# Optimization experiments

Measured on AMD Instinct MI355X. Metric: run time of the kernel, lower is better.

The kernel has to match this reference:

```python
import jax, jax.numpy as jnp
import numpy as np
import math

B = 2048
INPUT_SIZE = 1024
OUTPUT_SIZE = 512
SPONGE = 1024
ACT = 256
REC = 256
STORE = ACT + REC  # 512
DEPTH = 8
BDEPTH = 10
NEUTRAL_C = 1.0
SQRT2 = math.sqrt(2.0)


def _make_structure():
    # Deterministic stand-in for the module's random.sample-based recall wiring.
    rng = np.random.RandomState(0)
    half = (SPONGE + 1) // 2
    shuffle_perm = np.array([i // 2 + (i % 2) * half for i in range(SPONGE)], dtype=np.int64)
    unused = []
    recall = []
    for i in range(DEPTH):
        unused.extend(range(i * STORE, (i + 1) * STORE))
        sel = rng.choice(len(unused), size=REC, replace=False)
        sel_set = set(sel.tolist())
        recall.append([unused[k] for k in sorted(sel_set)])
        unused = [u for k, u in enumerate(unused) if k not in sel_set]
    out_mem = np.array(sorted(unused), dtype=np.int64)  # 2048 leftover memory columns
    bf_size = len(out_mem) + SPONGE  # 3072
    bf_depth = int(math.ceil(math.log2(bf_size)))  # 12
    bf_half = (bf_size + 1) // 2
    bf_perm = np.array([i // 2 + (i % 2) * bf_half for i in range(bf_size)], dtype=np.int64)
    return shuffle_perm, np.array(recall, dtype=np.int64), out_mem, bf_perm, bf_size, bf_depth


def setup_inputs() -> dict:
    key = jax.random.key(0)
    ks = jax.random.split(key, 6)
    shuffle_perm, recall_idx, out_mem_idx, bf_perm, bf_size, bf_depth = _make_structure()
    return {
        "X": jax.random.normal(ks[0], (B, INPUT_SIZE), jnp.float32),
        "scales": jnp.ones((INPUT_SIZE,), jnp.float32),
        "angles": jax.random.uniform(ks[1], (DEPTH, BDEPTH, SPONGE // 2), jnp.float32) * (2 * math.pi),
        "act_bias": jax.random.normal(ks[2], (DEPTH, ACT), jnp.float32),
        "act_activation": jax.random.normal(ks[3], (DEPTH, ACT), jnp.float32),
        "act_curvature": jax.random.normal(ks[4], (DEPTH, ACT), jnp.float32),
        "bf_angles": jax.random.uniform(ks[5], (bf_depth, bf_size // 2), jnp.float32) * (2 * math.pi),
        "shuffle_perm": jnp.asarray(shuffle_perm),
        "recall_idx": jnp.asarray(recall_idx),
        "output_mem_idx": jnp.asarray(out_mem_idx),
        "bf_perm": jnp.asarray(bf_perm),
    }


def _base_activation(x, c):
    # In the source, `a` is overwritten with torch.tensor(1.0), so a == 1.
    t = (math.pi / 4) / c
    y0 = (1.0 / c) * (1.0 / SQRT2 - math.cos(math.pi / 2))  # = 1/(c*sqrt(2))
    m0 = math.sin(math.pi / 2)  # = 1
    y1 = (1.0 / c) * (1.0 / SQRT2 - 1.0)
    m1 = math.sin(0.0)  # = 0
    mid = (1.0 / c) * (1.0 / SQRT2 - jnp.cos(math.pi / 4 + c * x))
    return jnp.where(x > t, y0 + m0 * (x - t), jnp.where(x < -t, y1 + m1 * (x + t), mid))


def _butterfly(x, angles, perm):
    # angles: [n_layers, exch]; shuffle -> Givens rotation per pair, extra passthrough
    exch = angles.shape[1]
    for j in range(angles.shape[0]):
        s = x[:, perm]
        x1, x2 = s[:, :exch], s[:, exch:2 * exch]
        ca, sa = jnp.cos(angles[j]), jnp.sin(angles[j])
        x = jnp.concatenate([ca * x1 + sa * x2, -sa * x1 + ca * x2, s[:, 2 * exch:]], axis=1)
    return x


def reference(X, scales, angles, act_bias, act_activation, act_curvature, bf_angles,
              shuffle_perm, recall_idx, output_mem_idx, bf_perm):
    Xs = X * scales
    sponge = Xs[:, :SPONGE]  # input_size == sponge_size: no zero pad, memory[0] is empty
    mem = jnp.zeros((Xs.shape[0], DEPTH * STORE), Xs.dtype)
    for i in range(DEPTH):
        sponge = _butterfly(sponge, angles[i], shuffle_perm)
        x1 = sponge[:, STORE:STORE + ACT] + act_bias[i]  # activation_position == store_size
        c = 0.5 * NEUTRAL_C * (act_curvature[i] + jnp.sqrt(act_curvature[i] ** 2 + 1.0))
        ap = _base_activation(x1, c)
        am = _base_activation(-x1, c)
        act_out = jnp.stack([ap, am], axis=2).reshape(ap.shape[0], 2 * ACT)  # interleave +/-
        mem = mem.at[:, i * STORE:(i + 1) * STORE].set(sponge[:, :STORE])
        recall = mem[:, recall_idx[i]]  # indices only address already-filled columns
        # [act_out | sponge[store:act_pos] (empty) | sponge[act_pos+ACT:] | recall]
        sponge = jnp.concatenate([act_out, sponge[:, STORE + ACT:], recall], axis=1)
    pre = jnp.concatenate([mem[:, output_mem_idx], sponge], axis=1)  # [B, 3072]
    out = _butterfly(pre, bf_angles, bf_perm)
    return out[:, :OUTPUT_SIZE]
```

## Files before the change

kernel.cpp:

```cpp
#include <hip/hip_runtime.h>
#include <math.h>

#define NB 2048
#define DEPTH 8

#define FTAB_OFF    0
#define BF01_OFF    81920
#define BFF_OFF     88064
#define ACT4_OFF    98304
#define PHYSA_OFF   106496
#define PHYSR_OFF   110592
#define PHYSO2_OFF  112640

#define MB0 4608
#define MB1 6656

__global__ void setup_kernel(const float* __restrict__ angles,
                             const float* __restrict__ bf_angles,
                             const float* __restrict__ act_bias,
                             const float* __restrict__ act_curv,
                             const int* __restrict__ recall_idx,
                             const int* __restrict__ out_mem_idx,
                             float* __restrict__ ws) {
    __shared__ int physL[4096];
    if (blockIdx.x < 200) {
        int id = blockIdx.x * 256 + threadIdx.x;
        if (id < 40960) {
            int w = id & 3, t = (id >> 2) & 255, dg = id >> 10;
            int d = dg / 5, g = dg - 5 * d;
            int a = 2 * (t & 127) + (t >> 7);
            int pair = (w == 0) ? a : (w == 1) ? (a + 256)
                     : (w == 2) ? (2 * a) : (2 * a + 1);
            int st = 2 * g + (w >> 1);
            float ang = angles[(d * 10 + st) * 512 + pair];
            float s, c; __sincosf(ang, &s, &c);
            ws[FTAB_OFF + 2 * id]     = c;
            ws[FTAB_OFF + 2 * id + 1] = s;
        } else if (id < 44032) {
            int e = id - 40960;
            int w = e & 3; int ti = e >> 2;
            int t = ti / 3; int i = ti - 3 * t;
            int a = t + 256 * i;
            int pair = (w == 0) ? a : (w == 1) ? (a + 768)
                     : (w == 2) ? (2 * a) : (2 * a + 1);
            int stage = (w < 2) ? 0 : 1;
            float ang = bf_angles[stage * 1536 + pair];
            float s, c; __sincosf(ang, &s, &c);
            ws[BF01_OFF + 2 * e]     = c;
            ws[BF01_OFF + 2 * e + 1] = s;
        } else if (id < 49152) {
            int e = id - 44032;
            int f = e >> 10; int rem = e & 1023; int t = rem >> 2; int w = rem & 3;
            int P;
            if (f == 0) P = 3 * t;
            else if (f < 4) { int k = 8 - 2 * f;
                              P = ((t >> (2 * f)) * (768 >> k)) + (t & ((256 >> k) - 1)); }
            else P = t;
            int pair = (w == 0) ? P : (w == 1) ? (P + 768)
                     : (w == 2) ? (2 * P) : (2 * P + 1);
            int stage = (w < 2) ? (2 + 2 * f) : (3 + 2 * f);
            float ang = bf_angles[stage * 1536 + pair];
            float s, c; __sincosf(ang, &s, &c);
            ws[BFF_OFF + 2 * e]     = c;
            ws[BFF_OFF + 2 * e + 1] = s;
        } else if (id < 51200) {
            int ida = id - 49152;
            float cu = act_curv[ida];
            float c  = 0.5f * (cu + sqrtf(cu * cu + 1.0f));
            ((float4*)(ws + ACT4_OFF))[ida] =
                make_float4(act_bias[ida], c, 1.0f / c, 0.0f);
        }
    } else {
        int tid = threadIdx.x;
        for (int e = tid; e < 4096; e += 256) {
            int v = e, p;
            for (;;) {
                int d = v >> 9, j = v & 511;
                if (d == 0)  { p = j; break; }
                if (j < 256) { p = 256 + d * 256 + j; break; }
                v = recall_idx[(d - 1) * 256 + (j - 256)];
            }
            physL[e] = p;
        }
        __syncthreads();
        int* pa = (int*)(ws + PHYSA_OFF);
        for (int e = tid; e < 2048; e += 256) {
            int d = e >> 8, t = e & 255;
            int a = 2 * (t & 127) + (t >> 7);
            pa[2 * e]     = 2 * physL[d * 512 + 2 * a];
            pa[2 * e + 1] = 2 * physL[d * 512 + 2 * a + 1];
        }
        int* pr = (int*)(ws + PHYSR_OFF);
        for (int e = tid; e < 2048; e += 256)
            pr[e] = 2 * physL[recall_idx[e]];
        int* po = (int*)(ws + PHYSO2_OFF);
        for (int e = tid; e < 3072; e += 256) {
            int tt = e / 12; int r = e - 12 * tt; int i = r >> 2; int k = r & 3;
            int a = tt + 256 * i;
            int tl2 = a >> 1, th2 = a & 1;
            int pos = tl2 + 1536 * th2 + 384 * k;
            po[e] = (pos < 2048) ? 2 * physL[out_mem_idx[pos]]
                                 : MB0 + 2 * (pos - 2048);
        }
    }
}

__device__ __forceinline__ float actf(float x, float c, float ic) {
    const float is2 = 0.70710678118654752f;
    float tt = 0.78539816339744831f * ic;
    float y0 = is2 * ic;
    float y1 = (is2 - 1.0f) * ic;
    float mid = ic * (is2 - __cosf(0.78539816339744831f + c * x));
    return x > tt ? (y0 + (x - tt)) : (x < -tt ? y1 : mid);
}

__launch_bounds__(256, 4)
__global__ void sponge_kernel(const float* __restrict__ X,
                              const float* __restrict__ scales,
                              const float* __restrict__ ws,
                              float* __restrict__ out) {
    __shared__ float L[8704];
    const int t = threadIdx.x;
    const int rowA = blockIdx.x * 2;

    const float4* bf01  = (const float4*)(ws + BF01_OFF);
    const float4* bff   = (const float4*)(ws + BFF_OFF);
    const float4* act4  = (const float4*)(ws + ACT4_OFF);
    const int2* physA  = (const int2*)(ws + PHYSA_OFF);
    const int*  physr  = (const int*)(ws + PHYSR_OFF);
    const int*  physo2 = (const int*)(ws + PHYSO2_OFF);

    const int tl = t & 127, th = t >> 7;
    const int b  = tl + th * 512;
    const int a  = 2 * tl + th;
    const int Wb = 2 * (tl & 15) + 32 * th + 64 * (tl >> 4);
    const int Rb = (tl & 1) + 2 * ((tl >> 2) & 15) + 32 * ((tl >> 1) & 1)
                 + 64 * (tl >> 6) + 512 * th;
    const int WI = 2 * Wb;
    const int RI = 2 * Rb;
    const int u  = t - 128;

    float hA0, hA1, hA2, hA3, hB0, hB1, hB2, hB3;
    {
        const float* Xr0 = X + (size_t)rowA * 1024;
        const float* Xr1 = Xr0 + 1024;
        float s0 = scales[b],       s1 = scales[b + 128];
        float s2 = scales[b + 256], s3 = scales[b + 384];
        hA0 = Xr0[b] * s0; hA1 = Xr0[b + 128] * s1;
        hA2 = Xr0[b + 256] * s2; hA3 = Xr0[b + 384] * s3;
        hB0 = Xr1[b] * s0; hB1 = Xr1[b + 128] * s1;
        hB2 = Xr1[b + 256] * s2; hB3 = Xr1[b + 384] * s3;
    }

    int woff = MB0, roff = MB1;
    const float4* ft = (const float4*)(ws + FTAB_OFF) + 2 * t;

#define DQUAD(cA, cB, i0, i1, i2, i3, F0, F1, F2, F3)                    \
    { float g0 =  (cA).x * (i0) + (cA).y * (i2);                         \
      float g2 = -(cA).y * (i0) + (cA).x * (i2);                         \
      float g1 =  (cA).z * (i1) + (cA).w * (i3);                         \
      float g3 = -(cA).w * (i1) + (cA).z * (i3);                         \
      F0 =  (cB).x * g0 + (cB).y * g1;                                   \
      F2 = -(cB).y * g0 + (cB).x * g1;                                   \
      F1 =  (cB).z * g2 + (cB).w * g3;                                   \
      F3 = -(cB).w * g2 + (cB).z * g3; }

    for (int d = 0; d < DEPTH; ++d) {
        for (int g = 0; g < 5; ++g) {
            float4 csA = ft[0], csB = ft[1]; ft += 512;
            float fA0, fA1, fA2, fA3, fB0, fB1, fB2, fB3;
            DQUAD(csA, csB, hA0, hA1, hA2, hA3, fA0, fA1, fA2, fA3);
            DQUAD(csA, csB, hB0, hB1, hB2, hB3, fB0, fB1, fB2, fB3);
            if (g < 4) {
                *(float4*)(L + woff + WI)        = make_float4(fA0, fB0, fA1, fB1);
                *(float4*)(L + woff + WI + 1024) = make_float4(fA2, fB2, fA3, fB3);
                { int tmp = woff; woff = roff; roff = tmp; }
                __syncthreads();
                float2 e0 = *(const float2*)(L + roff + RI);
                float2 e1 = *(const float2*)(L + roff + RI + 256);
                float2 e2 = *(const float2*)(L + roff + RI + 512);
                float2 e3 = *(const float2*)(L + roff + RI + 768);
                hA0 = e0.x; hB0 = e0.y; hA1 = e1.x; hB1 = e1.y;
                hA2 = e2.x; hB2 = e2.y; hA3 = e3.x; hB3 = e3.y;
            } else {
                int2 pm = physA[d * 256 + t];
                *(float2*)(L + pm.x) = make_float2(fA0, fB0);
                *(float2*)(L + pm.y) = make_float2(fA1, fB1);
                *(float4*)(L + woff + 4 * a) = make_float4(fA2, fB2, fA3, fB3);
                { int tmp = woff; woff = roff; roff = tmp; }
                int r0 = 0, r1 = 0;
                float4 a0, a1, a2, a3;
                if (t < 128) {
                    int k0 = t >> 1;
                    a0 = act4[d * 256 + k0];
                    a1 = act4[d * 256 + k0 + 64];
                    a2 = act4[d * 256 + k0 + 128];
                    a3 = act4[d * 256 + k0 + 192];
                } else {
                    r0 = physr[d * 256 + u];
                    r1 = physr[d * 256 + u + 128];
                }
                __syncthreads();
                const float* Z = L + roff;
                if (t < 128) {
                    int k0 = t >> 1;
                    float sgn = (t & 1) ? -1.0f : 1.0f;
                    float2 z0 = *(const float2*)(Z + 2 * k0);
                    float2 z1 = *(const float2*)(Z + 2 * k0 + 128);
                    float2 z2 = *(const float2*)(Z + 2 * k0 + 256);
                    float2 z3 = *(const float2*)(Z + 2 * k0 + 384);
                    hA0 = actf(sgn * (z0.x + a0.x), a0.y, a0.z);
                    hB0 = actf(sgn * (z0.y + a0.x), a0.y, a0.z);
                    hA1 = actf(sgn * (z1.x + a1.x), a1.y, a1.z);
                    hB1 = actf(sgn * (z1.y + a1.x), a1.y, a1.z);
                    hA2 = actf(sgn * (z2.x + a2.x), a2.y, a2.z);
                    hB2 = actf(sgn * (z2.y + a2.x), a2.y, a2.z);
                    hA3 = actf(sgn * (z3.x + a3.x), a3.y, a3.z);
                    hB3 = actf(sgn * (z3.y + a3.x), a3.y, a3.z);
                } else {
                    float2 k0v = *(const float2*)(Z + 512 + 2 * u);
                    float2 k1v = *(const float2*)(Z + 768 + 2 * u);
                    float2 rc0 = *(const float2*)(L + r0);
                    float2 rc1 = *(const float2*)(L + r1);
                    hA0 = k0v.x; hB0 = k0v.y;
                    hA1 = k1v.x; hB1 = k1v.y;
                    hA2 = rc0.x; hB2 = rc0.y;
                    hA3 = rc1.x; hB3 = rc1.y;
                }
            }
        }
    }

    *(float2*)(L + MB0 + 2 * b)       = make_float2(hA0, hB0);
    *(float2*)(L + MB0 + 2 * b + 256) = make_float2(hA1, hB1);
    *(float2*)(L + MB0 + 2 * b + 512) = make_float2(hA2, hB2);
    *(float2*)(L + MB0 + 2 * b + 768) = make_float2(hA3, hB3);
    __syncthreads();

    float2 w0, w1, w2, w3, w4, w5, w6, w7, w8, w9, w10, w11;
    {
        int4 pg = ((const int4*)(physo2 + t * 12))[0];
        w0 = *(const float2*)(L + pg.x); w1 = *(const float2*)(L + pg.y);
        w2 = *(const float2*)(L + pg.z); w3 = *(const float2*)(L + pg.w);
        pg = ((const int4*)(physo2 + t * 12))[1];
        w4 = *(const float2*)(L + pg.x); w5 = *(const float2*)(L + pg.y);
        w6 = *(const float2*)(L + pg.z); w7 = *(const float2*)(L + pg.w);
        pg = ((const int4*)(physo2 + t * 12))[2];
        w8 = *(const float2*)(L + pg.x); w9 = *(const float2*)(L + pg.y);
        w10 = *(const float2*)(L + pg.z); w11 = *(const float2*)(L + pg.w);
    }
    __syncthreads();

#define BF01_STEP(i, q0, q1, q2, q3)                                                \
    {                                                                               \
        float4 c01 = bf01[(t * 3 + (i)) * 2];                                       \
        float4 c23 = bf01[(t * 3 + (i)) * 2 + 1];                                   \
        float yA0, yA1, yA2, yA3, yB0, yB1, yB2, yB3;                               \
        DQUAD(c01, c23, q0.x, q1.x, q2.x, q3.x, yA0, yA1, yA2, yA3);                \
        DQUAD(c01, c23, q0.y, q1.y, q2.y, q3.y, yB0, yB1, yB2, yB3);                \
        *(float4*)(L + 4 * t + 1024 * (i))        = make_float4(yA0, yB0, yA1, yB1);\
        *(float4*)(L + 4 * t + 1024 * (i) + 3072) = make_float4(yA2, yB2, yA3, yB3);\
    }
    BF01_STEP(0, w0, w1, w2, w3)
    BF01_STEP(1, w4, w5, w6, w7)
    BF01_STEP(2, w8, w9, w10, w11)
#undef BF01_STEP
    __syncthreads();

#pragma unroll
    for (int f = 0; f < 4; ++f) {
        int P;
        if (f == 0) P = 3 * t;
        else { const int k = 8 - 2 * f;
               P = ((t >> (2 * f)) * (768 >> k)) + (t & ((256 >> k) - 1)); }
        int base = 2 * ((P >> 1) + (P & 1) * 1536);
        float4 csS = bff[(f * 256 + t) * 2];
        float4 csT = bff[(f * 256 + t) * 2 + 1];
        float2 x1p = *(const float2*)(L + base);
        float2 x1q = *(const float2*)(L + base + 768);
        float2 x2p = *(const float2*)(L + base + 1536);
        float2 x2q = *(const float2*)(L + base + 2304);
        float o1P =  csS.x * x1p.x + csS.y * x2p.x;
        float o2P = -csS.y * x1p.x + csS.x * x2p.x;
        float o1Q =  csS.z * x1q.x + csS.w * x2q.x;
        float o2Q = -csS.w * x1q.x + csS.z * x2q.x;
        float yA0 =  csT.x * o1P + csT.y * o1Q;
        float yA2 = -csT.y * o1P + csT.x * o1Q;
        float yA1 =  csT.z * o2P + csT.w * o2Q;
        float yA3 = -csT.w * o2P + csT.z * o2Q;
        o1P =  csS.x * x1p.y + csS.y * x2p.y;
        o2P = -csS.y * x1p.y + csS.x * x2p.y;
        o1Q =  csS.z * x1q.y + csS.w * x2q.y;
        o2Q = -csS.w * x1q.y + csS.z * x2q.y;
        float yB0 =  csT.x * o1P + csT.y * o1Q;
        float yB2 = -csT.y * o1P + csT.x * o1Q;
        float yB1 =  csT.z * o2P + csT.w * o2Q;
        float yB3 = -csT.w * o2P + csT.z * o2Q;
        __syncthreads();
        *(float4*)(L + 4 * P)        = make_float4(yA0, yB0, yA1, yB1);
        *(float4*)(L + 4 * P + 3072) = make_float4(yA2, yB2, yA3, yB3);
        __syncthreads();
    }

    {
        int base = 2 * ((t >> 1) + (t & 1) * 1536);
        float4 csS = bff[(4 * 256 + t) * 2];
        float4 csT = bff[(4 * 256 + t) * 2 + 1];
        float2 x1p = *(const float2*)(L + base);
        float2 x1q = *(const float2*)(L + base + 768);
        float2 x2p = *(const float2*)(L + base + 1536);
        float2 x2q = *(const float2*)(L + base + 2304);
        float o1P =  csS.x * x1p.x + csS.y * x2p.x;
        float o2P = -csS.y * x1p.x + csS.x * x2p.x;
        float o1Q =  csS.z * x1q.x + csS.w * x2q.x;
        float o2Q = -csS.w * x1q.x + csS.z * x2q.x;
        *(float2*)(out + (size_t)rowA * 512 + 2 * t) =
            make_float2(csT.x * o1P + csT.y * o1Q, csT.z * o2P + csT.w * o2Q);
        o1P =  csS.x * x1p.y + csS.y * x2p.y;
        o2P = -csS.y * x1p.y + csS.x * x2p.y;
        o1Q =  csS.z * x1q.y + csS.w * x2q.y;
        o2Q = -csS.w * x1q.y + csS.z * x2q.y;
        *(float2*)(out + (size_t)(rowA + 1) * 512 + 2 * t) =
            make_float2(csT.x * o1P + csT.y * o1Q, csT.z * o2P + csT.w * o2Q);
    }
#undef DQUAD
}

extern "C" void kernel_launch(void* const* d_in, const int* in_sizes, int n_in,
                              void* d_out, int out_size, void* d_ws, size_t ws_size,
                              hipStream_t stream) {
    const float* X          = (const float*)d_in[0];
    const float* scales     = (const float*)d_in[1];
    const float* angles     = (const float*)d_in[2];
    const float* act_bias   = (const float*)d_in[3];
    const float* act_curv   = (const float*)d_in[5];
    const float* bf_angles  = (const float*)d_in[6];
    const int*   recall_idx  = (const int*)d_in[8];
    const int*   out_mem_idx = (const int*)d_in[9];

    float* ws = (float*)d_ws;

    setup_kernel<<<201, 256, 0, stream>>>(angles, bf_angles, act_bias, act_curv,
                                          recall_idx, out_mem_idx, ws);
    sponge_kernel<<<NB / 2, 256, 0, stream>>>(X, scales, ws, (float*)d_out);
}
```

Before: 119.8 us.

## Run each row pair on a single wavefront to drop block barriers

Each row pair is now processed by one 64-lane wavefront instead of a 256-thread block. Each lane handles four virtual threads in registers, and every __syncthreads is replaced by an LDS waitcnt fence that relies on wave-level lockstep. The double-buffered exchange region is dropped, and the next-stage rotation coefficients are prefetched while the LDS shuffle is in flight. In exchange, each lane holds far more register state, and with only 1024 single-wave blocks there is less parallelism per CU, so occupancy and latency hiding may suffer.

```diff
diff --git a/kernel.cpp b/kernel.cpp
--- a/kernel.cpp
+++ b/kernel.cpp
@@ -13,7 +13,9 @@
 #define PHYSO2_OFF  112640
 
 #define MB0 4608
-#define MB1 6656
+#define EXB 4608
+
+#define WFENCE() asm volatile("s_waitcnt lgkmcnt(0)" ::: "memory")
 
 __global__ void setup_kernel(const float* __restrict__ angles,
                              const float* __restrict__ bf_angles,
@@ -114,46 +116,39 @@
     return x > tt ? (y0 + (x - tt)) : (x < -tt ? y1 : mid);
 }
 
-__launch_bounds__(256, 4)
+__launch_bounds__(64, 2)
 __global__ void sponge_kernel(const float* __restrict__ X,
                               const float* __restrict__ scales,
                               const float* __restrict__ ws,
                               float* __restrict__ out) {
-    __shared__ float L[8704];
-    const int t = threadIdx.x;
+    __shared__ float L[6656];
+    const int lane = threadIdx.x;
     const int rowA = blockIdx.x * 2;
 
-    const float4* bf01  = (const float4*)(ws + BF01_OFF);
-    const float4* bff   = (const float4*)(ws + BFF_OFF);
-    const float4* act4  = (const float4*)(ws + ACT4_OFF);
-    const int2* physA  = (const int2*)(ws + PHYSA_OFF);
-    const int*  physr  = (const int*)(ws + PHYSR_OFF);
-    const int*  physo2 = (const int*)(ws + PHYSO2_OFF);
-
-    const int tl = t & 127, th = t >> 7;
-    const int b  = tl + th * 512;
-    const int a  = 2 * tl + th;
-    const int Wb = 2 * (tl & 15) + 32 * th + 64 * (tl >> 4);
-    const int Rb = (tl & 1) + 2 * ((tl >> 2) & 15) + 32 * ((tl >> 1) & 1)
-                 + 64 * (tl >> 6) + 512 * th;
-    const int WI = 2 * Wb;
-    const int RI = 2 * Rb;
-    const int u  = t - 128;
-
-    float hA0, hA1, hA2, hA3, hB0, hB1, hB2, hB3;
+    const float4* ftab   = (const float4*)(ws + FTAB_OFF);
+    const float4* bf01   = (const float4*)(ws + BF01_OFF);
+    const float4* bff    = (const float4*)(ws + BFF_OFF);
+    const float4* act4   = (const float4*)(ws + ACT4_OFF);
+    const int2*   physA  = (const int2*)(ws + PHYSA_OFF);
+    const int*    physr  = (const int*)(ws + PHYSR_OFF);
+    const int*    physo2 = (const int*)(ws + PHYSO2_OFF);
+
+    float hA[4][4], hB[4][4];
     {
         const float* Xr0 = X + (size_t)rowA * 1024;
         const float* Xr1 = Xr0 + 1024;
-        float s0 = scales[b],       s1 = scales[b + 128];
-        float s2 = scales[b + 256], s3 = scales[b + 384];
-        hA0 = Xr0[b] * s0; hA1 = Xr0[b + 128] * s1;
-        hA2 = Xr0[b + 256] * s2; hA3 = Xr0[b + 384] * s3;
-        hB0 = Xr1[b] * s0; hB1 = Xr1[b + 128] * s1;
-        hB2 = Xr1[b + 256] * s2; hB3 = Xr1[b + 384] * s3;
-    }
-
-    int woff = MB0, roff = MB1;
-    const float4* ft = (const float4*)(ws + FTAB_OFF) + 2 * t;
+#pragma unroll
+        for (int q = 0; q < 4; ++q) {
+            int tq = lane + 64 * q;
+            int b  = (tq & 127) + (tq >> 7) * 512;
+#pragma unroll
+            for (int k = 0; k < 4; ++k) {
+                float s = scales[b + 128 * k];
+                hA[q][k] = Xr0[b + 128 * k] * s;
+                hB[q][k] = Xr1[b + 128 * k] * s;
+            }
+        }
+    }
 
 #define DQUAD(cA, cB, i0, i1, i2, i3, F0, F1, F2, F3)                    \
     { float g0 =  (cA).x * (i0) + (cA).y * (i2);                         \
@@ -165,165 +160,240 @@
       F1 =  (cB).z * g2 + (cB).w * g3;                                   \
       F3 = -(cB).w * g2 + (cB).z * g3; }
 
+    float4 cs[4][2];
+    int fb = 0;
+#define LOADC()                                                          \
+    { _Pragma("unroll")                                                  \
+      for (int q = 0; q < 4; ++q) {                                      \
+          int tq = lane + 64 * q;                                        \
+          cs[q][0] = ftab[fb + 2 * tq];                                  \
+          cs[q][1] = ftab[fb + 2 * tq + 1];                              \
+      } fb += 512; }
+
+    LOADC();
+
+#pragma unroll 1
     for (int d = 0; d < DEPTH; ++d) {
-        for (int g = 0; g < 5; ++g) {
-            float4 csA = ft[0], csB = ft[1]; ft += 512;
+        float4 av[2][4]; int pr2[2][2]; int2 pmv[4];
+#pragma unroll
+        for (int q = 0; q < 2; ++q) {
+            int k0 = (lane + 64 * q) >> 1;
+#pragma unroll
+            for (int j = 0; j < 4; ++j) av[q][j] = act4[d * 256 + k0 + 64 * j];
+            int u = lane + 64 * q;
+            pr2[q][0] = physr[d * 256 + u];
+            pr2[q][1] = physr[d * 256 + u + 128];
+        }
+#pragma unroll
+        for (int q = 0; q < 4; ++q) pmv[q] = physA[d * 256 + lane + 64 * q];
+
+        for (int g = 0; g < 4; ++g) {
+#pragma unroll
+            for (int q = 0; q < 4; ++q) {
+                int tq = lane + 64 * q;
+                int tl = tq & 127, th = tq >> 7;
+                int WI = 2 * (2 * (tl & 15) + 32 * th + 64 * (tl >> 4));
+                float fA0, fA1, fA2, fA3, fB0, fB1, fB2, fB3;
+                DQUAD(cs[q][0], cs[q][1], hA[q][0], hA[q][1], hA[q][2], hA[q][3],
+                      fA0, fA1, fA2, fA3);
+                DQUAD(cs[q][0], cs[q][1], hB[q][0], hB[q][1], hB[q][2], hB[q][3],
+                      fB0, fB1, fB2, fB3);
+                *(float4*)(L + EXB + WI)        = make_float4(fA0, fB0, fA1, fB1);
+                *(float4*)(L + EXB + WI + 1024) = make_float4(fA2, fB2, fA3, fB3);
+            }
+            WFENCE();
+            LOADC();
+#pragma unroll
+            for (int q = 0; q < 4; ++q) {
+                int tq = lane + 64 * q;
+                int tl = tq & 127, th = tq >> 7;
+                int RI = 2 * ((tl & 1) + 2 * ((tl >> 2) & 15) + 32 * ((tl >> 1) & 1)
+                             + 64 * (tl >> 6) + 512 * th);
+                float2 e0 = *(const float2*)(L + EXB + RI);
+                float2 e1 = *(const float2*)(L + EXB + RI + 256);
+                float2 e2 = *(const float2*)(L + EXB + RI + 512);
+                float2 e3 = *(const float2*)(L + EXB + RI + 768);
+                hA[q][0] = e0.x; hB[q][0] = e0.y; hA[q][1] = e1.x; hB[q][1] = e1.y;
+                hA[q][2] = e2.x; hB[q][2] = e2.y; hA[q][3] = e3.x; hB[q][3] = e3.y;
+            }
+            WFENCE();
+        }
+
+#pragma unroll
+        for (int q = 0; q < 4; ++q) {
+            int tq = lane + 64 * q;
+            int tl = tq & 127, th = tq >> 7;
+            int aq = 2 * tl + th;
             float fA0, fA1, fA2, fA3, fB0, fB1, fB2, fB3;
-            DQUAD(csA, csB, hA0, hA1, hA2, hA3, fA0, fA1, fA2, fA3);
-            DQUAD(csA, csB, hB0, hB1, hB2, hB3, fB0, fB1, fB2, fB3);
-            if (g < 4) {
-                *(float4*)(L + woff + WI)        = make_float4(fA0, fB0, fA1, fB1);
-                *(float4*)(L + woff + WI + 1024) = make_float4(fA2, fB2, fA3, fB3);
-                { int tmp = woff; woff = roff; roff = tmp; }
-                __syncthreads();
-                float2 e0 = *(const float2*)(L + roff + RI);
-                float2 e1 = *(const float2*)(L + roff + RI + 256);
-                float2 e2 = *(const float2*)(L + roff + RI + 512);
-                float2 e3 = *(const float2*)(L + roff + RI + 768);
-                hA0 = e0.x; hB0 = e0.y; hA1 = e1.x; hB1 = e1.y;
-                hA2 = e2.x; hB2 = e2.y; hA3 = e3.x; hB3 = e3.y;
-            } else {
-                int2 pm = physA[d * 256 + t];
-                *(float2*)(L + pm.x) = make_float2(fA0, fB0);
-                *(float2*)(L + pm.y) = make_float2(fA1, fB1);
-                *(float4*)(L + woff + 4 * a) = make_float4(fA2, fB2, fA3, fB3);
-                { int tmp = woff; woff = roff; roff = tmp; }
-                int r0 = 0, r1 = 0;
-                float4 a0, a1, a2, a3;
-                if (t < 128) {
-                    int k0 = t >> 1;
-                    a0 = act4[d * 256 + k0];
-                    a1 = act4[d * 256 + k0 + 64];
-                    a2 = act4[d * 256 + k0 + 128];
-                    a3 = act4[d * 256 + k0 + 192];
-                } else {
-                    r0 = physr[d * 256 + u];
-                    r1 = physr[d * 256 + u + 128];
-                }
-                __syncthreads();
-                const float* Z = L + roff;
-                if (t < 128) {
-                    int k0 = t >> 1;
-                    float sgn = (t & 1) ? -1.0f : 1.0f;
-                    float2 z0 = *(const float2*)(Z + 2 * k0);
-                    float2 z1 = *(const float2*)(Z + 2 * k0 + 128);
-                    float2 z2 = *(const float2*)(Z + 2 * k0 + 256);
-                    float2 z3 = *(const float2*)(Z + 2 * k0 + 384);
-                    hA0 = actf(sgn * (z0.x + a0.x), a0.y, a0.z);
-                    hB0 = actf(sgn * (z0.y + a0.x), a0.y, a0.z);
-                    hA1 = actf(sgn * (z1.x + a1.x), a1.y, a1.z);
-                    hB1 = actf(sgn * (z1.y + a1.x), a1.y, a1.z);
-                    hA2 = actf(sgn * (z2.x + a2.x), a2.y, a2.z);
-                    hB2 = actf(sgn * (z2.y + a2.x), a2.y, a2.z);
-                    hA3 = actf(sgn * (z3.x + a3.x), a3.y, a3.z);
-                    hB3 = actf(sgn * (z3.y + a3.x), a3.y, a3.z);
-                } else {
-                    float2 k0v = *(const float2*)(Z + 512 + 2 * u);
-                    float2 k1v = *(const float2*)(Z + 768 + 2 * u);
-                    float2 rc0 = *(const float2*)(L + r0);
-                    float2 rc1 = *(const float2*)(L + r1);
-                    hA0 = k0v.x; hB0 = k0v.y;
-                    hA1 = k1v.x; hB1 = k1v.y;
-                    hA2 = rc0.x; hB2 = rc0.y;
-                    hA3 = rc1.x; hB3 = rc1.y;
-                }
-            }
-        }
-    }
-
-    *(float2*)(L + MB0 + 2 * b)       = make_float2(hA0, hB0);
-    *(float2*)(L + MB0 + 2 * b + 256) = make_float2(hA1, hB1);
-    *(float2*)(L + MB0 + 2 * b + 512) = make_float2(hA2, hB2);
-    *(float2*)(L + MB0 + 2 * b + 768) = make_float2(hA3, hB3);
-    __syncthreads();
-
-    float2 w0, w1, w2, w3, w4, w5, w6, w7, w8, w9, w10, w11;
-    {
-        int4 pg = ((const int4*)(physo2 + t * 12))[0];
-        w0 = *(const float2*)(L + pg.x); w1 = *(const float2*)(L + pg.y);
-        w2 = *(const float2*)(L + pg.z); w3 = *(const float2*)(L + pg.w);
-        pg = ((const int4*)(physo2 + t * 12))[1];
-        w4 = *(const float2*)(L + pg.x); w5 = *(const float2*)(L + pg.y);
-        w6 = *(const float2*)(L + pg.z); w7 = *(const float2*)(L + pg.w);
-        pg = ((const int4*)(physo2 + t * 12))[2];
-        w8 = *(const float2*)(L + pg.x); w9 = *(const float2*)(L + pg.y);
-        w10 = *(const float2*)(L + pg.z); w11 = *(const float2*)(L + pg.w);
-    }
-    __syncthreads();
-
-#define BF01_STEP(i, q0, q1, q2, q3)                                                \
-    {                                                                               \
-        float4 c01 = bf01[(t * 3 + (i)) * 2];                                       \
-        float4 c23 = bf01[(t * 3 + (i)) * 2 + 1];                                   \
-        float yA0, yA1, yA2, yA3, yB0, yB1, yB2, yB3;                               \
-        DQUAD(c01, c23, q0.x, q1.x, q2.x, q3.x, yA0, yA1, yA2, yA3);                \
-        DQUAD(c01, c23, q0.y, q1.y, q2.y, q3.y, yB0, yB1, yB2, yB3);                \
-        *(float4*)(L + 4 * t + 1024 * (i))        = make_float4(yA0, yB0, yA1, yB1);\
-        *(float4*)(L + 4 * t + 1024 * (i) + 3072) = make_float4(yA2, yB2, yA3, yB3);\
-    }
-    BF01_STEP(0, w0, w1, w2, w3)
-    BF01_STEP(1, w4, w5, w6, w7)
-    BF01_STEP(2, w8, w9, w10, w11)
-#undef BF01_STEP
-    __syncthreads();
+            DQUAD(cs[q][0], cs[q][1], hA[q][0], hA[q][1], hA[q][2], hA[q][3],
+                  fA0, fA1, fA2, fA3);
+            DQUAD(cs[q][0], cs[q][1], hB[q][0], hB[q][1], hB[q][2], hB[q][3],
+                  fB0, fB1, fB2, fB3);
+            *(float2*)(L + pmv[q].x) = make_float2(fA0, fB0);
+            *(float2*)(L + pmv[q].y) = make_float2(fA1, fB1);
+            *(float4*)(L + EXB + 4 * aq) = make_float4(fA2, fB2, fA3, fB3);
+        }
+        WFENCE();
+        if (d < DEPTH - 1) LOADC();
+        {
+            const float* Z = L + EXB;
+#pragma unroll
+            for (int q = 0; q < 2; ++q) {
+                int tq = lane + 64 * q;
+                int k0 = tq >> 1;
+                float sgn = (tq & 1) ? -1.0f : 1.0f;
+                float2 z0 = *(const float2*)(Z + 2 * k0);
+                float2 z1 = *(const float2*)(Z + 2 * k0 + 128);
+                float2 z2 = *(const float2*)(Z + 2 * k0 + 256);
+                float2 z3 = *(const float2*)(Z + 2 * k0 + 384);
+                hA[q][0] = actf(sgn * (z0.x + av[q][0].x), av[q][0].y, av[q][0].z);
+                hB[q][0] = actf(sgn * (z0.y + av[q][0].x), av[q][0].y, av[q][0].z);
+                hA[q][1] = actf(sgn * (z1.x + av[q][1].x), av[q][1].y, av[q][1].z);
+                hB[q][1] = actf(sgn * (z1.y + av[q][1].x), av[q][1].y, av[q][1].z);
+                hA[q][2] = actf(sgn * (z2.x + av[q][2].x), av[q][2].y, av[q][2].z);
+                hB[q][2] = actf(sgn * (z2.y + av[q][2].x), av[q][2].y, av[q][2].z);
+                hA[q][3] = actf(sgn * (z3.x + av[q][3].x), av[q][3].y, av[q][3].z);
+                hB[q][3] = actf(sgn * (z3.y + av[q][3].x), av[q][3].y, av[q][3].z);
+            }
+#pragma unroll
+            for (int q = 0; q < 2; ++q) {
+                int u = lane + 64 * q;
+                float2 k0v = *(const float2*)(Z + 512 + 2 * u);
+                float2 k1v = *(const float2*)(Z + 768 + 2 * u);
+                float2 rc0 = *(const float2*)(L + pr2[q][0]);
+                float2 rc1 = *(const float2*)(L + pr2[q][1]);
+                hA[2 + q][0] = k0v.x; hB[2 + q][0] = k0v.y;
+                hA[2 + q][1] = k1v.x; hB[2 + q][1] = k1v.y;
+                hA[2 + q][2] = rc0.x; hB[2 + q][2] = rc0.y;
+                hA[2 + q][3] = rc1.x; hB[2 + q][3] = rc1.y;
+            }
+        }
+        WFENCE();
+    }
+
+    int4 pga[4][3];
+#pragma unroll
+    for (int q = 0; q < 4; ++q) {
+        const int4* pgp = (const int4*)(physo2 + (lane + 64 * q) * 12);
+#pragma unroll
+        for (int j = 0; j < 3; ++j) pga[q][j] = pgp[j];
+    }
+#pragma unroll
+    for (int q = 0; q < 4; ++q) {
+        int tq = lane + 64 * q;
+        int b  = (tq & 127) + (tq >> 7) * 512;
+        *(float2*)(L + EXB + 2 * b)       = make_float2(hA[q][0], hB[q][0]);
+        *(float2*)(L + EXB + 2 * b + 256) = make_float2(hA[q][1], hB[q][1]);
+        *(float2*)(L + EXB + 2 * b + 512) = make_float2(hA[q][2], hB[q][2]);
+        *(float2*)(L + EXB + 2 * b + 768) = make_float2(hA[q][3], hB[q][3]);
+    }
+    WFENCE();
+
+    float2 w[4][12];
+#pragma unroll
+    for (int q = 0; q < 4; ++q) {
+        int4 pg = pga[q][0];
+        w[q][0] = *(const float2*)(L + pg.x); w[q][1] = *(const float2*)(L + pg.y);
+        w[q][2] = *(const float2*)(L + pg.z); w[q][3] = *(const float2*)(L + pg.w);
+        pg = pga[q][1];
+        w[q][4] = *(const float2*)(L + pg.x); w[q][5] = *(const float2*)(L + pg.y);
+        w[q][6] = *(const float2*)(L + pg.z); w[q][7] = *(const float2*)(L + pg.w);
+        pg = pga[q][2];
+        w[q][8]  = *(const float2*)(L + pg.x); w[q][9]  = *(const float2*)(L + pg.y);
+        w[q][10] = *(const float2*)(L + pg.z); w[q][11] = *(const float2*)(L + pg.w);
+    }
+    WFENCE();
+
+#pragma unroll
+    for (int q = 0; q < 4; ++q) {
+        int tq = lane + 64 * q;
+#pragma unroll
+        for (int i = 0; i < 3; ++i) {
+            float4 c01 = bf01[(tq * 3 + i) * 2];
+            float4 c23 = bf01[(tq * 3 + i) * 2 + 1];
+            float yA0, yA1, yA2, yA3, yB0, yB1, yB2, yB3;
+            DQUAD(c01, c23, w[q][4*i].x, w[q][4*i+1].x, w[q][4*i+2].x, w[q][4*i+3].x,
+                  yA0, yA1, yA2, yA3);
+            DQUAD(c01, c23, w[q][4*i].y, w[q][4*i+1].y, w[q][4*i+2].y, w[q][4*i+3].y,
+                  yB0, yB1, yB2, yB3);
+            *(float4*)(L + 4 * tq + 1024 * i)        = make_float4(yA0, yB0, yA1, yB1);
+            *(float4*)(L + 4 * tq + 1024 * i + 3072) = make_float4(yA2, yB2, yA3, yB3);
+        }
+    }
+    WFENCE();
 
 #pragma unroll
     for (int f = 0; f < 4; ++f) {
-        int P;
-        if (f == 0) P = 3 * t;
-        else { const int k = 8 - 2 * f;
-               P = ((t >> (2 * f)) * (768 >> k)) + (t & ((256 >> k) - 1)); }
-        int base = 2 * ((P >> 1) + (P & 1) * 1536);
-        float4 csS = bff[(f * 256 + t) * 2];
-        float4 csT = bff[(f * 256 + t) * 2 + 1];
+        float2 x1p[4], x1r[4], x2p[4], x2r[4];
+        float4 cS[4], cT[4];
+        int Pq[4];
+#pragma unroll
+        for (int q = 0; q < 4; ++q) {
+            int tq = lane + 64 * q;
+            cS[q] = bff[(f * 256 + tq) * 2];
+            cT[q] = bff[(f * 256 + tq) * 2 + 1];
+            int P;
+            if (f == 0) P = 3 * tq;
+            else { const int k = 8 - 2 * f;
+                   P = ((tq >> (2 * f)) * (768 >> k)) + (tq & ((256 >> k) - 1)); }
+            Pq[q] = P;
+            int base = 2 * ((P >> 1) + (P & 1) * 1536);
+            x1p[q] = *(const float2*)(L + base);
+            x1r[q] = *(const float2*)(L + base + 768);
+            x2p[q] = *(const float2*)(L + base + 1536);
+            x2r[q] = *(const float2*)(L + base + 2304);
+        }
+        WFENCE();
+#pragma unroll
+        for (int q = 0; q < 4; ++q) {
+            float4 csS = cS[q], csT = cT[q];
+            float o1P =  csS.x * x1p[q].x + csS.y * x2p[q].x;
+            float o2P = -csS.y * x1p[q].x + csS.x * x2p[q].x;
+            float o1Q =  csS.z * x1r[q].x + csS.w * x2r[q].x;
+            float o2Q = -csS.w * x1r[q].x + csS.z * x2r[q].x;
+            float yA0 =  csT.x * o1P + csT.y * o1Q;
+            float yA2 = -csT.y * o1P + csT.x * o1Q;
+            float yA1 =  csT.z * o2P + csT.w * o2Q;
+            float yA3 = -csT.w * o2P + csT.z * o2Q;
+            o1P =  csS.x * x1p[q].y + csS.y * x2p[q].y;
+            o2P = -csS.y * x1p[q].y + csS.x * x2p[q].y;
+            o1Q =  csS.z * x1r[q].y + csS.w * x2r[q].y;
+            o2Q = -csS.w * x1r[q].y + csS.z * x2r[q].y;
+            float yB0 =  csT.x * o1P + csT.y * o1Q;
+            float yB2 = -csT.y * o1P + csT.x * o1Q;
+            float yB1 =  csT.z * o2P + csT.w * o2Q;
+            float yB3 = -csT.w * o2P + csT.z * o2Q;
+            *(float4*)(L + 4 * Pq[q])        = make_float4(yA0, yB0, yA1, yB1);
+            *(float4*)(L + 4 * Pq[q] + 3072) = make_float4(yA2, yB2, yA3, yB3);
+        }
+        WFENCE();
+    }
+
+#pragma unroll
+    for (int q = 0; q < 4; ++q) {
+        int tq = lane + 64 * q;
+        int base = 2 * ((tq >> 1) + (tq & 1) * 1536);
+        float4 csS = bff[(4 * 256 + tq) * 2];
+        float4 csT = bff[(4 * 256 + tq) * 2 + 1];
         float2 x1p = *(const float2*)(L + base);
-        float2 x1q = *(const float2*)(L + base + 768);
+        float2 x1r = *(const float2*)(L + base + 768);
         float2 x2p = *(const float2*)(L + base + 1536);
-        float2 x2q = *(const float2*)(L + base + 2304);
+        float2 x2r = *(const float2*)(L + base + 2304);
         float o1P =  csS.x * x1p.x + csS.y * x2p.x;
         float o2P = -csS.y * x1p.x + csS.x * x2p.x;
-        float o1Q =  csS.z * x1q.x + csS.w * x2q.x;
-        float o2Q = -csS.w * x1q.x + csS.z * x2q.x;
-        float yA0 =  csT.x * o1P + csT.y * o1Q;
-        float yA2 = -csT.y * o1P + csT.x * o1Q;
-        float yA1 =  csT.z * o2P + csT.w * o2Q;
-        float yA3 = -csT.w * o2P + csT.z * o2Q;
-        o1P =  csS.x * x1p.y + csS.y * x2p.y;
-        o2P = -csS.y * x1p.y + csS.x * x2p.y;
-        o1Q =  csS.z * x1q.y + csS.w * x2q.y;
-        o2Q = -csS.w * x1q.y + csS.z * x2q.y;
-        float yB0 =  csT.x * o1P + csT.y * o1Q;
-        float yB2 = -csT.y * o1P + csT.x * o1Q;
-        float yB1 =  csT.z * o2P + csT.w * o2Q;
-        float yB3 = -csT.w * o2P + csT.z * o2Q;
-        __syncthreads();
-        *(float4*)(L + 4 * P)        = make_float4(yA0, yB0, yA1, yB1);
-        *(float4*)(L + 4 * P + 3072) = make_float4(yA2, yB2, yA3, yB3);
-        __syncthreads();
-    }
-
-    {
-        int base = 2 * ((t >> 1) + (t & 1) * 1536);
-        float4 csS = bff[(4 * 256 + t) * 2];
-        float4 csT = bff[(4 * 256 + t) * 2 + 1];
-        float2 x1p = *(const float2*)(L + base);
-        float2 x1q = *(const float2*)(L + base + 768);
-        float2 x2p = *(const float2*)(L + base + 1536);
-        float2 x2q = *(const float2*)(L + base + 2304);
-        float o1P =  csS.x * x1p.x + csS.y * x2p.x;
-        float o2P = -csS.y * x1p.x + csS.x * x2p.x;
-        float o1Q =  csS.z * x1q.x + csS.w * x2q.x;
-        float o2Q = -csS.w * x1q.x + csS.z * x2q.x;
-        *(float2*)(out + (size_t)rowA * 512 + 2 * t) =
+        float o1Q =  csS.z * x1r.x + csS.w * x2r.x;
+        float o2Q = -csS.w * x1r.x + csS.z * x2r.x;
+        *(float2*)(out + (size_t)rowA * 512 + 2 * tq) =
             make_float2(csT.x * o1P + csT.y * o1Q, csT.z * o2P + csT.w * o2Q);
         o1P =  csS.x * x1p.y + csS.y * x2p.y;
         o2P = -csS.y * x1p.y + csS.x * x2p.y;
-        o1Q =  csS.z * x1q.y + csS.w * x2q.y;
-        o2Q = -csS.w * x1q.y + csS.z * x2q.y;
-        *(float2*)(out + (size_t)(rowA + 1) * 512 + 2 * t) =
+        o1Q =  csS.z * x1r.y + csS.w * x2r.y;
+        o2Q = -csS.w * x1r.y + csS.z * x2r.y;
+        *(float2*)(out + (size_t)(rowA + 1) * 512 + 2 * tq) =
             make_float2(csT.x * o1P + csT.y * o1Q, csT.z * o2P + csT.w * o2Q);
     }
 #undef DQUAD
+#undef LOADC
 }
 
 extern "C" void kernel_launch(void* const* d_in, const int* in_sizes, int n_in,
@@ -342,5 +412,5 @@
 
     setup_kernel<<<201, 256, 0, stream>>>(angles, bf_angles, act_bias, act_curv,
                                           recall_idx, out_mem_idx, ws);
-    sponge_kernel<<<NB / 2, 256, 0, stream>>>(X, scales, ws, (float*)d_out);
+    sponge_kernel<<<NB / 2, 64, 0, stream>>>(X, scales, ws, (float*)d_out);
 }
```

Result: slower. 134.1 us (+11.9%).
